# Kernel optimization log

Hardware: AMD Instinct MI355X
Metric: run time of the kernel (lower is better)

## Reference

```python
import jax, jax.numpy as jnp
import numpy as np


def setup_inputs() -> dict:
    key = jax.random.key(0)
    k1, k2 = jax.random.split(key)
    B, BINS = 262144, 256
    x = jax.random.uniform(k1, (B, BINS), dtype=jnp.float32)
    y = jax.random.uniform(k2, (B, BINS), dtype=jnp.float32)
    return {"x": x, "y": y}


def reference(x, y):
    # torch: tt[i, j] = (j >= i), so x @ tt == cumulative sum of x along bins.
    # We replace the O(bins^2) triangular matmul with an O(bins) prefix scan.
    cdf_x = jnp.cumsum(x, axis=1)
    cdf_y = jnp.cumsum(y, axis=1)
    return jnp.sum(jnp.square(cdf_x - cdf_y), axis=1)
```

## Files before the change

kernel.cpp:

```cpp
#include <hip/hip_runtime.h>
#include <hip/hip_bf16.h>


__global__ __launch_bounds__(256) void emd_loss_kernel(
    const float* __restrict__ x,
    const float* __restrict__ y,
    float* __restrict__ out,
    int nrows) {
  const int lane = threadIdx.x & 63;
  const int wave_in_block = threadIdx.x >> 6;
  const int waves_per_block = blockDim.x >> 6;
  const int wave0 = blockIdx.x * waves_per_block + wave_in_block;
  const int nwaves = gridDim.x * waves_per_block;

  for (int row = wave0; row < nrows; row += nwaves) {
    const size_t base = (size_t)row * 256;
    const float4 xv = reinterpret_cast<const float4*>(x + base)[lane];
    const float4 yv = reinterpret_cast<const float4*>(y + base)[lane];

    const float d0 = xv.x - yv.x;
    const float d1 = xv.y - yv.y;
    const float d2 = xv.z - yv.z;
    const float d3 = xv.w - yv.w;

    const float p0 = d0;
    const float p1 = p0 + d1;
    const float p2 = p1 + d2;
    const float p3 = p2 + d3;

    float t = p3;
#pragma unroll
    for (int off = 1; off < 64; off <<= 1) {
      float v = __shfl_up(t, off, 64);
      if (lane >= off) t += v;
    }
    const float excl = t - p3;

    const float s0 = excl + p0;
    const float s1 = excl + p1;
    const float s2 = excl + p2;
    const float s3 = excl + p3;

    float acc = s0 * s0 + s1 * s1 + s2 * s2 + s3 * s3;

#pragma unroll
    for (int off = 32; off > 0; off >>= 1) acc += __shfl_xor(acc, off, 64);

    if (lane == 0) out[row] = acc;
  }
}

extern "C" void kernel_launch(void* const* d_in, const int* in_sizes, int n_in,
                              void* d_out, int out_size, void* d_ws, size_t ws_size,
                              hipStream_t stream) {
  const float* x = (const float*)d_in[0];
  const float* y = (const float*)d_in[1];
  float* out = (float*)d_out;
  const int nrows = in_sizes[0] / 256;

  const int block = 256;
  const int grid = 2048;
  emd_loss_kernel<<<grid, block, 0, stream>>>(x, y, out, nrows);
}
```

Baseline: 502.8 us.

## Assign one row per thread with serial scan instead of wave-per-row shuffles

```diff
diff --git a/kernel.cpp b/kernel.cpp
--- a/kernel.cpp
+++ b/kernel.cpp
@@ -2,52 +2,33 @@
 #include <hip/hip_bf16.h>
 
 
-__global__ __launch_bounds__(256) void emd_loss_kernel(
+__global__ __launch_bounds__(256) void emd_loss_rowthread(
     const float* __restrict__ x,
     const float* __restrict__ y,
     float* __restrict__ out,
     int nrows) {
-  const int lane = threadIdx.x & 63;
-  const int wave_in_block = threadIdx.x >> 6;
-  const int waves_per_block = blockDim.x >> 6;
-  const int wave0 = blockIdx.x * waves_per_block + wave_in_block;
-  const int nwaves = gridDim.x * waves_per_block;
+  const int row = blockIdx.x * blockDim.x + threadIdx.x;
+  if (row >= nrows) return;
 
-  for (int row = wave0; row < nrows; row += nwaves) {
-    const size_t base = (size_t)row * 256;
-    const float4 xv = reinterpret_cast<const float4*>(x + base)[lane];
-    const float4 yv = reinterpret_cast<const float4*>(y + base)[lane];
+  const float4* __restrict__ xr =
+      reinterpret_cast<const float4*>(x + (size_t)row * 256);
+  const float4* __restrict__ yr =
+      reinterpret_cast<const float4*>(y + (size_t)row * 256);
 
-    const float d0 = xv.x - yv.x;
-    const float d1 = xv.y - yv.y;
-    const float d2 = xv.z - yv.z;
-    const float d3 = xv.w - yv.w;
+  float s = 0.0f;
+  float acc = 0.0f;
 
-    const float p0 = d0;
-    const float p1 = p0 + d1;
-    const float p2 = p1 + d2;
-    const float p3 = p2 + d3;
+#pragma unroll 8
+  for (int k = 0; k < 64; ++k) {
+    const float4 xv = xr[k];
+    const float4 yv = yr[k];
+    s += xv.x - yv.x; acc = fmaf(s, s, acc);
+    s += xv.y - yv.y; acc = fmaf(s, s, acc);
+    s += xv.z - yv.z; acc = fmaf(s, s, acc);
+    s += xv.w - yv.w; acc = fmaf(s, s, acc);
+  }
 
-    float t = p3;
-#pragma unroll
-    for (int off = 1; off < 64; off <<= 1) {
-      float v = __shfl_up(t, off, 64);
-      if (lane >= off) t += v;
-    }
-    const float excl = t - p3;
-
-    const float s0 = excl + p0;
-    const float s1 = excl + p1;
-    const float s2 = excl + p2;
-    const float s3 = excl + p3;
-
-    float acc = s0 * s0 + s1 * s1 + s2 * s2 + s3 * s3;
-
-#pragma unroll
-    for (int off = 32; off > 0; off >>= 1) acc += __shfl_xor(acc, off, 64);
-
-    if (lane == 0) out[row] = acc;
-  }
+  out[row] = acc;
 }
 
 extern "C" void kernel_launch(void* const* d_in, const int* in_sizes, int n_in,
@@ -59,6 +40,6 @@
   const int nrows = in_sizes[0] / 256;
 
   const int block = 256;
-  const int grid = 2048;
-  emd_loss_kernel<<<grid, block, 0, stream>>>(x, y, out, nrows);
+  const int grid = (nrows + block - 1) / block;
+  emd_loss_rowthread<<<grid, block, 0, stream>>>(x, y, out, nrows);
 }
```

Measured after the change: 525.2 us. 1.04x slower.
